# Performance work log

Hardware: AMD Instinct MI355X
Metric: run time of the kernel (lower is better)

## Reference

```python
import jax, jax.numpy as jnp
import numpy as np

B, N, DIN, K, DS = 64, 4096, 256, 20, 64
NUM_ITERS = 3
EPS = 1e-8       # slot-attention eps
EPS_LN = 1e-5    # torch LayerNorm default eps


def _ln(x, g, b):
    m = x.mean(-1, keepdims=True)
    v = ((x - m) ** 2).mean(-1, keepdims=True)
    return (x - m) / jnp.sqrt(v + EPS_LN) * g + b


def setup_inputs() -> dict:
    key = jax.random.key(0)
    ks = jax.random.split(key, 12)
    s = 0.02
    return {
        "inputs": jax.random.normal(ks[0], (B, N, DIN), jnp.float32),
        "slot_noise": jax.random.normal(ks[1], (B, K, DS), jnp.float32),
        "slot_mu": jax.random.normal(ks[2], (1, 1, DS), jnp.float32),
        "slot_log_sigma": jnp.zeros((1, 1, DS), jnp.float32),
        "ln_in_g": jnp.ones((DIN,), jnp.float32),
        "ln_in_b": jnp.zeros((DIN,), jnp.float32),
        "Wk": jax.random.normal(ks[3], (DIN, DS), jnp.float32) * s,
        "Wv": jax.random.normal(ks[4], (DIN, DS), jnp.float32) * s,
        "Wq": jax.random.normal(ks[5], (DS, DS), jnp.float32) * s,
        "ln_slot_g": jnp.ones((DS,), jnp.float32),
        "ln_slot_b": jnp.zeros((DS,), jnp.float32),
        "gru_Wih": jax.random.normal(ks[6], (3 * DS, DS), jnp.float32) * s,
        "gru_Whh": jax.random.normal(ks[7], (3 * DS, DS), jnp.float32) * s,
        "gru_bih": jnp.zeros((3 * DS,), jnp.float32),
        "gru_bhh": jnp.zeros((3 * DS,), jnp.float32),
        "ln_mlp_g": jnp.ones((DS,), jnp.float32),
        "ln_mlp_b": jnp.zeros((DS,), jnp.float32),
        "mlp_W1": jax.random.normal(ks[8], (DS, 4 * DS), jnp.float32) * s,
        "mlp_b1": jnp.zeros((4 * DS,), jnp.float32),
        "mlp_W2": jax.random.normal(ks[9], (4 * DS, DS), jnp.float32) * s,
        "mlp_b2": jnp.zeros((DS,), jnp.float32),
    }


def reference(inputs, slot_noise, slot_mu, slot_log_sigma, ln_in_g, ln_in_b,
              Wk, Wv, Wq, ln_slot_g, ln_slot_b,
              gru_Wih, gru_Whh, gru_bih, gru_bhh,
              ln_mlp_g, ln_mlp_b, mlp_W1, mlp_b1, mlp_W2, mlp_b2):
    x = _ln(inputs, ln_in_g, ln_in_b)            # (B, N, DIN)
    k = x @ Wk                                    # (B, N, DS)
    v = x @ Wv                                    # (B, N, DS)
    slots = slot_mu + jnp.exp(slot_log_sigma) * slot_noise  # (B, K, DS)
    scale = DS ** -0.5
    attn = None
    for _ in range(NUM_ITERS):
        slots_prev = slots
        q = _ln(slots, ln_slot_g, ln_slot_b) @ Wq                # (B, K, DS)
        dots = jnp.einsum('bkd,bnd->bkn', q, k) * scale          # (B, K, N)
        attn = jax.nn.softmax(dots, axis=1)                      # softmax over slots
        attn_norm = attn / (attn.sum(-1, keepdims=True) + EPS)
        updates = jnp.einsum('bkn,bnd->bkd', attn_norm, v)       # (B, K, DS)
        # torch GRUCell: gates ordered r, z, n
        gi = updates @ gru_Wih.T + gru_bih
        gh = slots_prev @ gru_Whh.T + gru_bhh
        i_r, i_z, i_n = jnp.split(gi, 3, axis=-1)
        h_r, h_z, h_n = jnp.split(gh, 3, axis=-1)
        r = jax.nn.sigmoid(i_r + h_r)
        z = jax.nn.sigmoid(i_z + h_z)
        n = jnp.tanh(i_n + r * h_n)
        slots = (1.0 - z) * n + z * slots_prev
        h = _ln(slots, ln_mlp_g, ln_mlp_b)
        slots = slots + (jax.nn.relu(h @ mlp_W1 + mlp_b1) @ mlp_W2 + mlp_b2)
    return slots, attn
```

## Files before the change

kernel.cpp:

```cpp
#include <hip/hip_runtime.h>
#include <cstdint>
#include <cstddef>

using f32x4  = __attribute__((ext_vector_type(4))) float;
using bf16x8 = __attribute__((ext_vector_type(8))) short;

__device__ __forceinline__ unsigned short f2bf(float f){
  unsigned int u = __float_as_uint(f);
  return (unsigned short)((u + 0x7fffu + ((u >> 16) & 1u)) >> 16);
}

#define SWZ(o)    ((o) ^ ((((o) >> 9) & 7) << 4))
#define SWZ128(o) ((o) ^ ((((o) >> 7) & 7) << 4))

__global__ __launch_bounds__(256) void k_prep(
    const float* __restrict__ Wk, const float* __restrict__ Wv,
    const float* __restrict__ Wih, const float* __restrict__ Whh,
    const float* __restrict__ W1,  const float* __restrict__ W2,
    const float* __restrict__ Wq,
    const float* __restrict__ noise, const float* __restrict__ mu,
    const float* __restrict__ lsig,
    const float* __restrict__ lsg, const float* __restrict__ lsb,
    unsigned short* __restrict__ PWt,
    unsigned short* __restrict__ PWih, unsigned short* __restrict__ PWhh,
    unsigned short* __restrict__ PW1T, unsigned short* __restrict__ PW2T,
    unsigned short* __restrict__ PWq,
    float* __restrict__ slots, float* __restrict__ qws){
  const int bx = blockIdx.x, t = threadIdx.x;
  if (bx < 128){
    int idx = bx * 256 + t;
    int e = idx & 7, lane = (idx >> 3) & 63, f = idx >> 9;
    int pass = f >> 5, brT = (f >> 3) & 3, kk = f & 7;
    int n_loc = brT * 16 + (lane & 15);
    int c = kk * 32 + (lane >> 4) * 8 + e;
    const float* src = pass ? Wv : Wk;
    PWt[idx] = f2bf(src[c * 64 + n_loc]);
    return;
  }
  if (bx < 368){
    int idx = (bx - 128) * 256 + t;
    int rel, kstN;
    const float* src; unsigned short* dst; int mode;
    if (idx < 12288)      { rel = idx;          kstN = 2; src = Wih; dst = PWih; mode = 0; }
    else if (idx < 24576) { rel = idx - 12288;  kstN = 2; src = Whh; dst = PWhh; mode = 0; }
    else if (idx < 40960) { rel = idx - 24576;  kstN = 2; src = W1;  dst = PW1T; mode = 1; }
    else if (idx < 57344) { rel = idx - 40960;  kstN = 8; src = W2;  dst = PW2T; mode = 2; }
    else                  { rel = idx - 57344;  kstN = 2; src = Wq;  dst = PWq;  mode = 3; }
    int e = rel & 7, lane = (rel >> 3) & 63, f = rel >> 9;
    int jt = f / kstN, kst = f - jt * kstN;
    int row = jt * 16 + (lane & 15);
    int col = kst * 32 + (lane >> 4) * 8 + e;
    float v;
    if (mode == 0)      v = src[row * 64 + col];
    else if (mode == 1) v = src[col * 256 + row];
    else if (mode == 2) v = src[col * 64 + row];
    else                v = src[col * 64 + row];
    dst[rel] = f2bf(v);
    return;
  }
  {
    __shared__ __align__(16) float xsh[4][64];
    int idx = bx - 368;
    int d = t & 63, w4 = t >> 6;
    int bk = idx * 4 + w4;
    float s = mu[d] + __expf(lsig[d]) * noise[bk * 64 + d];
    slots[bk * 64 + d] = s;
    float s1 = s, s2 = s * s;
    #pragma unroll
    for (int off = 32; off >= 1; off >>= 1){
      s1 += __shfl_xor(s1, off);
      s2 += __shfl_xor(s2, off);
    }
    float m = s1 * (1.f / 64.f);
    float var = s2 * (1.f / 64.f) - m * m;
    float rstd = rsqrtf(var + 1e-5f);
    float xn = (s - m) * rstd * lsg[d] + lsb[d];
    xsh[w4][d] = xn;
    __syncthreads();
    float q = 0.f;
    #pragma unroll
    for (int i = 0; i < 64; ++i) q += xsh[w4][i] * Wq[i * 64 + d];
    qws[bk * 64 + d] = q;
  }
}

__global__ __launch_bounds__(256) void k_lnkv(
    const float* __restrict__ x, const float* __restrict__ lng, const float* __restrict__ lnb,
    const unsigned short* __restrict__ PWt,
    unsigned short* __restrict__ kbF, unsigned short* __restrict__ vF){
  extern __shared__ char smem[];
  char* As = smem;
  char* Cs = smem + 16384;
  const int t = threadIdx.x;
  const int lane = t & 63, w = t >> 6;
  const int gm0 = blockIdx.x * 32;

  const float4 g4 = *(const float4*)(lng + lane * 4);
  const float4 b4 = *(const float4*)(lnb + lane * 4);

  {
    float4 xv[8];
    #pragma unroll
    for (int j = 0; j < 8; ++j){
      int r = w * 8 + j;
      xv[j] = *(const float4*)(x + (size_t)(gm0 + r) * 256 + lane * 4);
    }
    #pragma unroll
    for (int j = 0; j < 8; ++j){
      int r = w * 8 + j;
      float4 v = xv[j];
      float s  = v.x + v.y + v.z + v.w;
      float s2 = v.x * v.x + v.y * v.y + v.z * v.z + v.w * v.w;
      #pragma unroll
      for (int off = 32; off >= 1; off >>= 1){
        s  += __shfl_xor(s,  off);
        s2 += __shfl_xor(s2, off);
      }
      float mean = s * (1.f / 256.f);
      float var  = s2 * (1.f / 256.f) - mean * mean;
      float rstd = rsqrtf(var + 1e-5f);
      unsigned int p0 = (unsigned)f2bf((v.x - mean) * rstd * g4.x + b4.x) |
                        ((unsigned)f2bf((v.y - mean) * rstd * g4.y + b4.y) << 16);
      unsigned int p1 = (unsigned)f2bf((v.z - mean) * rstd * g4.z + b4.z) |
                        ((unsigned)f2bf((v.w - mean) * rstd * g4.w + b4.w) << 16);
      int off8 = r * 512 + lane * 8;
      *(uint2*)(As + SWZ(off8)) = make_uint2(p0, p1);
    }
  }
  __syncthreads();

  const int wm = w >> 1, wn = w & 1;
  const int l15 = lane & 15, l4 = lane >> 4;

  #pragma unroll 1
  for (int pass = 0; pass < 2; ++pass){
    f32x4 acc[2];
    acc[0] = (f32x4){0.f,0.f,0.f,0.f};
    acc[1] = (f32x4){0.f,0.f,0.f,0.f};

    #pragma unroll
    for (int kk = 0; kk < 8; ++kk){
      int ar = wm * 16 + l15;
      bf16x8 a = *(const bf16x8*)(As + SWZ(ar * 512 + kk * 64 + l4 * 16));
      bf16x8 bfr[2];
      #pragma unroll
      for (int j = 0; j < 2; ++j){
        int f = pass * 32 + (wn * 2 + j) * 8 + kk;
        bfr[j] = *(const bf16x8*)(PWt + ((size_t)(f * 64 + lane)) * 8);
      }
      #pragma unroll
      for (int j = 0; j < 2; ++j)
        acc[j] = __builtin_amdgcn_mfma_f32_16x16x32_bf16(a, bfr[j], acc[j], 0, 0, 0);
    }
    if (pass == 1) __syncthreads();

    #pragma unroll
    for (int j = 0; j < 2; ++j)
      #pragma unroll
      for (int reg = 0; reg < 4; ++reg){
        int row = wm * 16 + l4 * 4 + reg;
        int colb = ((wn * 2 + j) * 16 + l15) * 2;
        *(unsigned short*)(Cs + row * 128 + (colb ^ ((row & 7) << 4))) = f2bf(acc[j][reg]);
      }
    __syncthreads();

    if (pass == 0){
      const int lo = t & 63, kst = (t >> 6) & 1, nt = t >> 7;
      int row = nt * 16 + (lo & 15);
      int colb = (kst * 32 + (lo >> 4) * 8) * 2;
      uint4 val = *(const uint4*)(Cs + row * 128 + (colb ^ ((row & 7) << 4)));
      size_t ntile = (size_t)blockIdx.x * 2 + nt;
      *(uint4*)(kbF + (ntile * 2 + kst) * 512 + lo * 8) = val;
    } else {
      const size_t chunkF = (size_t)(gm0 >> 7);
      const int kstG = (gm0 >> 5) & 3;
      const int dtile = t >> 6;
      unsigned short ev[8];
      #pragma unroll
      for (int e = 0; e < 8; ++e){
        int row = (lane >> 4) * 8 + e;
        int colb = (dtile * 16 + (lane & 15)) * 2;
        ev[e] = *(const unsigned short*)(Cs + row * 128 + (colb ^ ((row & 7) << 4)));
      }
      *(uint4*)(vF + ((chunkF * 4 + dtile) * 4 + kstG) * 512 + lane * 8) = *(const uint4*)ev;
    }
  }
}

__global__ __launch_bounds__(256) void k_attn2(
    const unsigned short* __restrict__ kbF, const unsigned short* __restrict__ vF,
    const float* __restrict__ qws, float* __restrict__ Spart, float* __restrict__ Upart,
    float* __restrict__ attn_out, int write_attn){
  __shared__ __align__(16) char sm[12672];
  char* qs  = sm;
  char* Ps  = sm + 4096;
  float* sred = (float*)(sm + 12288);
  const int t = threadIdx.x, lane = t & 63, w = t >> 6;
  const int l15 = lane & 15, g = lane >> 4;
  const int b = blockIdx.y, chunk = blockIdx.x, n0 = chunk * 128;

  if (t < 160){
    int r = t >> 3, c = t & 7;
    const float4* qp = (const float4*)(qws + (size_t)b * 1280 + r * 64 + c * 8);
    float4 a0 = qp[0], a1 = qp[1];
    uint4 pk;
    pk.x = (unsigned)f2bf(a0.x) | ((unsigned)f2bf(a0.y) << 16);
    pk.y = (unsigned)f2bf(a0.z) | ((unsigned)f2bf(a0.w) << 16);
    pk.z = (unsigned)f2bf(a1.x) | ((unsigned)f2bf(a1.y) << 16);
    pk.w = (unsigned)f2bf(a1.z) | ((unsigned)f2bf(a1.w) << 16);
    *(uint4*)(qs + r * 128 + ((c * 16) ^ ((r & 7) << 4))) = pk;
  }
  __syncthreads();

  f32x4 c2[2][2];
  #pragma unroll
  for (int kt = 0; kt < 2; ++kt)
    #pragma unroll
    for (int nt = 0; nt < 2; ++nt)
      c2[kt][nt] = (f32x4){0.f, 0.f, 0.f, 0.f};
  #pragma unroll
  for (int kst = 0; kst < 2; ++kst){
    bf16x8 aq[2], bk2[2];
    #pragma unroll
    for (int kt = 0; kt < 2; ++kt){
      int row = kt * 16 + l15;
      aq[kt] = *(const bf16x8*)(qs + row * 128 + ((kst * 64 + g * 16) ^ ((row & 7) << 4)));
    }
    #pragma unroll
    for (int nt = 0; nt < 2; ++nt){
      size_t ntile = (size_t)b * 256 + chunk * 8 + w * 2 + nt;
      bk2[nt] = *(const bf16x8*)(kbF + (ntile * 2 + kst) * 512 + lane * 8);
    }
    #pragma unroll
    for (int kt = 0; kt < 2; ++kt)
      #pragma unroll
      for (int nt = 0; nt < 2; ++nt)
        c2[kt][nt] = __builtin_amdgcn_mfma_f32_16x16x32_bf16(aq[kt], bk2[nt], c2[kt][nt], 0, 0, 0);
  }

  float p[2][2][4];
  #pragma unroll
  for (int kt = 0; kt < 2; ++kt)
    #pragma unroll
    for (int nt = 0; nt < 2; ++nt)
      #pragma unroll
      for (int reg = 0; reg < 4; ++reg)
        p[kt][nt][reg] = c2[kt][nt][reg] * 0.125f;
  if (g){
    #pragma unroll
    for (int nt = 0; nt < 2; ++nt)
      #pragma unroll
      for (int reg = 0; reg < 4; ++reg)
        p[1][nt][reg] = -1e30f;
  }

  #pragma unroll
  for (int nt = 0; nt < 2; ++nt){
    float mx = p[0][nt][0];
    #pragma unroll
    for (int reg = 1; reg < 4; ++reg) mx = fmaxf(mx, p[0][nt][reg]);
    #pragma unroll
    for (int reg = 0; reg < 4; ++reg) mx = fmaxf(mx, p[1][nt][reg]);
    mx = fmaxf(mx, __shfl_xor(mx, 16));
    mx = fmaxf(mx, __shfl_xor(mx, 32));
    float s = 0.f;
    #pragma unroll
    for (int kt = 0; kt < 2; ++kt)
      #pragma unroll
      for (int reg = 0; reg < 4; ++reg){
        float e = __expf(p[kt][nt][reg] - mx);
        p[kt][nt][reg] = e; s += e;
      }
    s += __shfl_xor(s, 16);
    s += __shfl_xor(s, 32);
    float inv = 1.f / s;
    #pragma unroll
    for (int kt = 0; kt < 2; ++kt)
      #pragma unroll
      for (int reg = 0; reg < 4; ++reg)
        p[kt][nt][reg] *= inv;
  }

  {
    float sr[2][4];
    #pragma unroll
    for (int kt = 0; kt < 2; ++kt)
      #pragma unroll
      for (int reg = 0; reg < 4; ++reg)
        sr[kt][reg] = p[kt][0][reg] + p[kt][1][reg];
    #pragma unroll
    for (int off = 1; off <= 8; off <<= 1)
      #pragma unroll
      for (int kt = 0; kt < 2; ++kt)
        #pragma unroll
        for (int reg = 0; reg < 4; ++reg)
          sr[kt][reg] += __shfl_xor(sr[kt][reg], off);
    if (l15 == 0){
      #pragma unroll
      for (int kt = 0; kt < 2; ++kt)
        #pragma unroll
        for (int reg = 0; reg < 4; ++reg){
          int ks = kt * 16 + g * 4 + reg;
          if (ks < 20) sred[ks * 4 + w] = sr[kt][reg];
        }
    }
  }

  if (write_attn){
    #pragma unroll
    for (int kt = 0; kt < 2; ++kt)
      #pragma unroll
      for (int nt = 0; nt < 2; ++nt)
        #pragma unroll
        for (int reg = 0; reg < 4; ++reg){
          int ks = kt * 16 + g * 4 + reg;
          if (ks < 20)
            attn_out[((size_t)(b * 20 + ks)) * 4096 + n0 + w * 32 + nt * 16 + l15] = p[kt][nt][reg];
        }
  }

  #pragma unroll
  for (int kt = 0; kt < 2; ++kt)
    #pragma unroll
    for (int nt = 0; nt < 2; ++nt)
      #pragma unroll
      for (int reg = 0; reg < 4; ++reg){
        int row = kt * 16 + g * 4 + reg;
        int colb = (w * 32 + nt * 16 + l15) * 2;
        *(unsigned short*)(Ps + row * 256 + (colb ^ ((row & 7) << 4))) = f2bf(p[kt][nt][reg]);
      }
  __syncthreads();

  if (t < 20)
    Spart[((size_t)b * 20 + t) * 32 + chunk] =
        sred[t * 4 + 0] + sred[t * 4 + 1] + sred[t * 4 + 2] + sred[t * 4 + 3];

  f32x4 u[2];
  u[0] = (f32x4){0.f,0.f,0.f,0.f};
  u[1] = (f32x4){0.f,0.f,0.f,0.f};
  #pragma unroll
  for (int kst = 0; kst < 4; ++kst){
    bf16x8 pa[2], bv;
    #pragma unroll
    for (int kt = 0; kt < 2; ++kt){
      int row = kt * 16 + l15;
      pa[kt] = *(const bf16x8*)(Ps + row * 256 + ((kst * 64 + g * 16) ^ ((row & 7) << 4)));
    }
    bv = *(const bf16x8*)(vF + ((((size_t)b * 32 + chunk) * 4 + w) * 4 + kst) * 512 + lane * 8);
    #pragma unroll
    for (int kt = 0; kt < 2; ++kt)
      u[kt] = __builtin_amdgcn_mfma_f32_16x16x32_bf16(pa[kt], bv, u[kt], 0, 0, 0);
  }
  #pragma unroll
  for (int kt = 0; kt < 2; ++kt)
    #pragma unroll
    for (int reg = 0; reg < 4; ++reg){
      int ks = kt * 16 + g * 4 + reg;
      if (ks < 20)
        Upart[((size_t)(b * 32 + chunk) * 20 + ks) * 64 + w * 16 + l15] = u[kt][reg];
    }
}

__global__ __launch_bounds__(1024) void k_slot(
    float* __restrict__ slots, const float* __restrict__ Upart, const float* __restrict__ Spart,
    const unsigned short* __restrict__ PWih, const unsigned short* __restrict__ PWhh,
    const unsigned short* __restrict__ PW1T, const unsigned short* __restrict__ PW2T,
    const unsigned short* __restrict__ PWq,
    const float* __restrict__ bih, const float* __restrict__ bhh,
    const float* __restrict__ b1, const float* __restrict__ b2,
    const float* __restrict__ lmg, const float* __restrict__ lmb,
    const float* __restrict__ lsg, const float* __restrict__ lsb,
    float* __restrict__ qws, float* __restrict__ out_slots, int last){
  extern __shared__ char sm[];
  float* g1f = (float*)sm;
  float* g2f = g1f + 192 * 33;
  char*  reluT = sm;
  char*  ubf   = sm + 50688;
  char*  sbfb  = sm + 54784;
  char*  hbf   = sm + 58880;
  char*  sqbf  = sm + 62976;
  float* snewF = (float*)(sm + 67072);
  float* prevF = (float*)(sm + 75392);
  float* sfinF = (float*)(sm + 83712);
  float* sSr   = (float*)(sm + 92032);

  const int t = threadIdx.x, lane = t & 63, wv = t >> 6;
  const int l15 = lane & 15, g4 = lane >> 4;
  const int b = blockIdx.x;

  if (t < 20){
    const float* sp = Spart + ((size_t)b * 20 + t) * 32;
    float ss = 0.f;
    #pragma unroll
    for (int c = 0; c < 32; ++c) ss += sp[c];
    sSr[t] = 1.f / (ss + 1e-8f);
  }
  __syncthreads();

  #pragma unroll
  for (int i = 0; i < 2; ++i){
    int idx = t + 1024 * i;
    if (idx < 1280){
      int m = idx >> 6, d = idx & 63;
      const float* up = Upart + (size_t)b * 40960 + m * 64 + d;
      float uv = 0.f;
      #pragma unroll
      for (int c = 0; c < 32; ++c) uv += up[(size_t)c * 1280];
      uv *= sSr[m];
      float pv = slots[((size_t)b * 20 + m) * 64 + d];
      int off = m * 128 + d * 2;
      *(unsigned short*)(ubf  + SWZ128(off)) = f2bf(uv);
      *(unsigned short*)(sbfb + SWZ128(off)) = f2bf(pv);
      prevF[m * 65 + d] = pv;
    }
  }
  __syncthreads();

  {
    const int which = wv >> 3, mg = (wv >> 2) & 1, jg = wv & 3;
    const unsigned short* PA = which ? PWhh : PWih;
    const char* Bt = which ? sbfb : ubf;
    float* gout = which ? g2f : g1f;
    f32x4 acc[3];
    #pragma unroll
    for (int jj = 0; jj < 3; ++jj) acc[jj] = (f32x4){0.f,0.f,0.f,0.f};
    #pragma unroll
    for (int kst = 0; kst < 2; ++kst){
      int roff = (mg * 16 + l15) * 128 + (kst * 32 + g4 * 8) * 2;
      bf16x8 bfrag = *(const bf16x8*)(Bt + SWZ128(roff));
      #pragma unroll
      for (int jj = 0; jj < 3; ++jj){
        int jt = jg * 3 + jj;
        bf16x8 afrag = *(const bf16x8*)(PA + ((size_t)((jt * 2 + kst) * 64 + lane)) * 8);
        acc[jj] = __builtin_amdgcn_mfma_f32_16x16x32_bf16(afrag, bfrag, acc[jj], 0, 0, 0);
      }
    }
    #pragma unroll
    for (int jj = 0; jj < 3; ++jj){
      int jt = jg * 3 + jj;
      #pragma unroll
      for (int reg = 0; reg < 4; ++reg)
        gout[(jt * 16 + g4 * 4 + reg) * 33 + mg * 16 + l15] = acc[jj][reg];
    }
  }
  __syncthreads();

  {
    const int d = lane;
    const float bi_r = bih[d], bi_z = bih[64 + d], bi_n = bih[128 + d];
    const float bh_r = bhh[d], bh_z = bhh[64 + d], bh_n = bhh[128 + d];
    const float lg = lmg[d], lb = lmb[d];
    #pragma unroll
    for (int mi = 0; mi < 2; ++mi){
      int m = wv + mi * 16;
      if (m < 20){
        float i_r = g1f[d * 33 + m] + bi_r;
        float i_z = g1f[(64 + d) * 33 + m] + bi_z;
        float i_n = g1f[(128 + d) * 33 + m] + bi_n;
        float h_r = g2f[d * 33 + m] + bh_r;
        float h_z = g2f[(64 + d) * 33 + m] + bh_z;
        float h_n = g2f[(128 + d) * 33 + m] + bh_n;
        float r = 1.f / (1.f + __expf(-(i_r + h_r)));
        float z = 1.f / (1.f + __expf(-(i_z + h_z)));
        float nn = tanhf(i_n + r * h_n);
        float pv = prevF[m * 65 + d];
        float sn = (1.f - z) * nn + z * pv;
        snewF[m * 65 + d] = sn;
        float s1 = sn, s2 = sn * sn;
        #pragma unroll
        for (int off = 32; off >= 1; off >>= 1){
          s1 += __shfl_xor(s1, off);
          s2 += __shfl_xor(s2, off);
        }
        float mean = s1 * (1.f / 64.f);
        float var = s2 * (1.f / 64.f) - mean * mean;
        float rstd = rsqrtf(var + 1e-5f);
        float h = (sn - mean) * rstd * lg + lb;
        *(unsigned short*)(hbf + SWZ128(m * 128 + d * 2)) = f2bf(h);
      }
    }
  }
  __syncthreads();

  {
    const int jt = wv;
    f32x4 acc[2];
    acc[0] = (f32x4){0.f,0.f,0.f,0.f};
    acc[1] = (f32x4){0.f,0.f,0.f,0.f};
    #pragma unroll
    for (int kst = 0; kst < 2; ++kst){
      bf16x8 afrag = *(const bf16x8*)(PW1T + ((size_t)((jt * 2 + kst) * 64 + lane)) * 8);
      #pragma unroll
      for (int mg = 0; mg < 2; ++mg){
        int roff = (mg * 16 + l15) * 128 + (kst * 32 + g4 * 8) * 2;
        bf16x8 bh2 = *(const bf16x8*)(hbf + SWZ128(roff));
        acc[mg] = __builtin_amdgcn_mfma_f32_16x16x32_bf16(afrag, bh2, acc[mg], 0, 0, 0);
      }
    }
    #pragma unroll
    for (int reg = 0; reg < 4; ++reg){
      int j = jt * 16 + g4 * 4 + reg;
      float bb = b1[j];
      #pragma unroll
      for (int mg = 0; mg < 2; ++mg){
        float vv = fmaxf(acc[mg][reg] + bb, 0.f);
        int m = mg * 16 + l15;
        int off = m * 512 + j * 2;
        *(unsigned short*)(reluT + SWZ(off)) = f2bf(vv);
      }
    }
  }
  __syncthreads();

  if (wv < 8){
    const int dd = wv >> 1, mg = wv & 1;
    f32x4 acc = (f32x4){0.f,0.f,0.f,0.f};
    #pragma unroll
    for (int kst = 0; kst < 8; ++kst){
      bf16x8 afrag = *(const bf16x8*)(PW2T + ((size_t)((dd * 8 + kst) * 64 + lane)) * 8);
      int row = mg * 16 + l15;
      int off = row * 512 + (kst * 32 + g4 * 8) * 2;
      bf16x8 bfrag = *(const bf16x8*)(reluT + SWZ(off));
      acc = __builtin_amdgcn_mfma_f32_16x16x32_bf16(afrag, bfrag, acc, 0, 0, 0);
    }
    #pragma unroll
    for (int reg = 0; reg < 4; ++reg){
      int m = mg * 16 + l15;
      int dcol = dd * 16 + g4 * 4 + reg;
      if (m < 20){
        float sf = snewF[m * 65 + dcol] + acc[reg] + b2[dcol];
        sfinF[m * 65 + dcol] = sf;
        slots[((size_t)b * 20 + m) * 64 + dcol] = sf;
        if (last) out_slots[((size_t)b * 20 + m) * 64 + dcol] = sf;
      }
    }
  }
  if (last) return;
  __syncthreads();

  {
    const int d = lane;
    const float lg = lsg[d], lb = lsb[d];
    #pragma unroll
    for (int mi = 0; mi < 2; ++mi){
      int m = wv + mi * 16;
      if (m < 20){
        float sv = sfinF[m * 65 + d];
        float s1 = sv, s2 = sv * sv;
        #pragma unroll
        for (int off = 32; off >= 1; off >>= 1){
          s1 += __shfl_xor(s1, off);
          s2 += __shfl_xor(s2, off);
        }
        float mean = s1 * (1.f / 64.f);
        float var = s2 * (1.f / 64.f) - mean * mean;
        float rstd = rsqrtf(var + 1e-5f);
        float xn = (sv - mean) * rstd * lg + lb;
        *(unsigned short*)(sqbf + SWZ128(m * 128 + d * 2)) = f2bf(xn);
      }
    }
  }
  __syncthreads();
  if (wv < 8){
    const int jt = wv >> 1, mg = wv & 1;
    f32x4 acc = (f32x4){0.f,0.f,0.f,0.f};
    #pragma unroll
    for (int kst = 0; kst < 2; ++kst){
      bf16x8 afrag = *(const bf16x8*)(PWq + ((size_t)((jt * 2 + kst) * 64 + lane)) * 8);
      int roff = (mg * 16 + l15) * 128 + (kst * 32 + g4 * 8) * 2;
      bf16x8 bfrag = *(const bf16x8*)(sqbf + SWZ128(roff));
      acc = __builtin_amdgcn_mfma_f32_16x16x32_bf16(afrag, bfrag, acc, 0, 0, 0);
    }
    #pragma unroll
    for (int reg = 0; reg < 4; ++reg){
      int m = mg * 16 + l15;
      int j = jt * 16 + g4 * 4 + reg;
      if (m < 20) qws[(size_t)b * 1280 + m * 64 + j] = acc[reg];
    }
  }
}

extern "C" void kernel_launch(void* const* d_in, const int* in_sizes, int n_in,
                              void* d_out, int out_size, void* d_ws, size_t ws_size,
                              hipStream_t stream){
  const float* inputs = (const float*)d_in[0];
  const float* noise  = (const float*)d_in[1];
  const float* mu     = (const float*)d_in[2];
  const float* lsig   = (const float*)d_in[3];
  const float* ln_in_g= (const float*)d_in[4];
  const float* ln_in_b= (const float*)d_in[5];
  const float* Wk     = (const float*)d_in[6];
  const float* Wv     = (const float*)d_in[7];
  const float* Wq     = (const float*)d_in[8];
  const float* ln_s_g = (const float*)d_in[9];
  const float* ln_s_b = (const float*)d_in[10];
  const float* Wih    = (const float*)d_in[11];
  const float* Whh    = (const float*)d_in[12];
  const float* bih    = (const float*)d_in[13];
  const float* bhh    = (const float*)d_in[14];
  const float* lmg    = (const float*)d_in[15];
  const float* lmb    = (const float*)d_in[16];
  const float* W1     = (const float*)d_in[17];
  const float* b1     = (const float*)d_in[18];
  const float* W2     = (const float*)d_in[19];
  const float* b2     = (const float*)d_in[20];

  char* ws = (char*)d_ws;
  unsigned short* kbF = (unsigned short*)ws;
  unsigned short* vF  = (unsigned short*)(ws + 33554432);
  unsigned short* PWt = (unsigned short*)(ws + 67108864);
  float* slots        = (float*)(ws + 67174400);
  float* qws          = (float*)(ws + 67502080);
  float* Upart        = (float*)(ws + 67829760);
  float* Spart        = (float*)(ws + 78315520);
  unsigned short* PWih= (unsigned short*)(ws + 78479360);
  unsigned short* PWhh= (unsigned short*)(ws + 78503936);
  unsigned short* PW1T= (unsigned short*)(ws + 78528512);
  unsigned short* PW2T= (unsigned short*)(ws + 78561280);
  unsigned short* PWq = (unsigned short*)(ws + 78594048);

  float* slots_out = (float*)d_out;
  float* attn_out  = slots_out + 81920;

  hipLaunchKernelGGL(k_prep, dim3(688), dim3(256), 0, stream,
                     Wk, Wv, Wih, Whh, W1, W2, Wq, noise, mu, lsig, ln_s_g, ln_s_b,
                     PWt, PWih, PWhh, PW1T, PW2T, PWq, slots, qws);
  hipLaunchKernelGGL(k_lnkv, dim3(8192), dim3(256), 20480, stream, inputs, ln_in_g, ln_in_b,
                     PWt, kbF, vF);

  for (int it = 0; it < 3; ++it){
    hipLaunchKernelGGL(k_attn2, dim3(32, 64), dim3(256), 0, stream, kbF, vF, qws, Spart, Upart,
                       attn_out, (it == 2) ? 1 : 0);
    hipLaunchKernelGGL(k_slot, dim3(64), dim3(1024), 92160, stream, slots, Upart, Spart,
                       PWih, PWhh, PW1T, PW2T, PWq, bih, bhh, b1, b2,
                       lmg, lmb, ln_s_g, ln_s_b, qws, slots_out, (it == 2) ? 1 : 0);
  }
}
```

Before: 164.4 us.

## Replace per-chunk partial sums with atomic accumulation and fold small prep into lnkv

The attention kernel now accumulates slot sums and updates with float atomicAdd into a compact per-batch buffer instead of writing 32 per-chunk partials, and the slot kernel reads and zeroes that buffer. This removes the 32-way partial reduction reads in k_slot and the large partial-buffer traffic. The GRU/MLP weight packing and initial slot/q computation move into extra blocks of the k_lnkv launch, so the prep kernel becomes small and also zeroes the accumulators. Atomics add contention (32 chunks per address) and make the summation order nondeterministic.

```diff
diff --git a/kernel.cpp b/kernel.cpp
--- a/kernel.cpp
+++ b/kernel.cpp
@@ -15,85 +15,93 @@
 
 __global__ __launch_bounds__(256) void k_prep(
     const float* __restrict__ Wk, const float* __restrict__ Wv,
+    unsigned short* __restrict__ PWt, float* __restrict__ Uacc ){
+  const int bx = blockIdx.x, t = threadIdx.x;
+  int idx = bx * 256 + t;
+  int e = idx & 7, lane = (idx >> 3) & 63, f = idx >> 9;
+  int pass = f >> 5, brT = (f >> 3) & 3, kk = f & 7;
+  int n_loc = brT * 16 + (lane & 15);
+  int c = kk * 32 + (lane >> 4) * 8 + e;
+  const float* src = pass ? Wv : Wk;
+  PWt[idx] = f2bf(src[c * 64 + n_loc]);
+  #pragma unroll
+  for (int i = 0; i < 3; ++i){
+    int z = idx + 32768 * i;
+    if (z < 83200) Uacc[z] = 0.f;
+  }
+}
+
+__global__ __launch_bounds__(256) void k_lnkv(
+    const float* __restrict__ x, const float* __restrict__ lng, const float* __restrict__ lnb,
+    const unsigned short* __restrict__ PWt,
+    unsigned short* __restrict__ kbF, unsigned short* __restrict__ vF,
     const float* __restrict__ Wih, const float* __restrict__ Whh,
     const float* __restrict__ W1,  const float* __restrict__ W2,
     const float* __restrict__ Wq,
     const float* __restrict__ noise, const float* __restrict__ mu,
     const float* __restrict__ lsig,
     const float* __restrict__ lsg, const float* __restrict__ lsb,
-    unsigned short* __restrict__ PWt,
     unsigned short* __restrict__ PWih, unsigned short* __restrict__ PWhh,
     unsigned short* __restrict__ PW1T, unsigned short* __restrict__ PW2T,
     unsigned short* __restrict__ PWq,
     float* __restrict__ slots, float* __restrict__ qws){
-  const int bx = blockIdx.x, t = threadIdx.x;
-  if (bx < 128){
-    int idx = bx * 256 + t;
-    int e = idx & 7, lane = (idx >> 3) & 63, f = idx >> 9;
-    int pass = f >> 5, brT = (f >> 3) & 3, kk = f & 7;
-    int n_loc = brT * 16 + (lane & 15);
-    int c = kk * 32 + (lane >> 4) * 8 + e;
-    const float* src = pass ? Wv : Wk;
-    PWt[idx] = f2bf(src[c * 64 + n_loc]);
-    return;
-  }
-  if (bx < 368){
-    int idx = (bx - 128) * 256 + t;
-    int rel, kstN;
-    const float* src; unsigned short* dst; int mode;
-    if (idx < 12288)      { rel = idx;          kstN = 2; src = Wih; dst = PWih; mode = 0; }
-    else if (idx < 24576) { rel = idx - 12288;  kstN = 2; src = Whh; dst = PWhh; mode = 0; }
-    else if (idx < 40960) { rel = idx - 24576;  kstN = 2; src = W1;  dst = PW1T; mode = 1; }
-    else if (idx < 57344) { rel = idx - 40960;  kstN = 8; src = W2;  dst = PW2T; mode = 2; }
-    else                  { rel = idx - 57344;  kstN = 2; src = Wq;  dst = PWq;  mode = 3; }
-    int e = rel & 7, lane = (rel >> 3) & 63, f = rel >> 9;
-    int jt = f / kstN, kst = f - jt * kstN;
-    int row = jt * 16 + (lane & 15);
-    int col = kst * 32 + (lane >> 4) * 8 + e;
-    float v;
-    if (mode == 0)      v = src[row * 64 + col];
-    else if (mode == 1) v = src[col * 256 + row];
-    else if (mode == 2) v = src[col * 64 + row];
-    else                v = src[col * 64 + row];
-    dst[rel] = f2bf(v);
-    return;
-  }
-  {
-    __shared__ __align__(16) float xsh[4][64];
-    int idx = bx - 368;
-    int d = t & 63, w4 = t >> 6;
-    int bk = idx * 4 + w4;
-    float s = mu[d] + __expf(lsig[d]) * noise[bk * 64 + d];
-    slots[bk * 64 + d] = s;
-    float s1 = s, s2 = s * s;
-    #pragma unroll
-    for (int off = 32; off >= 1; off >>= 1){
-      s1 += __shfl_xor(s1, off);
-      s2 += __shfl_xor(s2, off);
-    }
-    float m = s1 * (1.f / 64.f);
-    float var = s2 * (1.f / 64.f) - m * m;
-    float rstd = rsqrtf(var + 1e-5f);
-    float xn = (s - m) * rstd * lsg[d] + lsb[d];
-    xsh[w4][d] = xn;
-    __syncthreads();
-    float q = 0.f;
-    #pragma unroll
-    for (int i = 0; i < 64; ++i) q += xsh[w4][i] * Wq[i * 64 + d];
-    qws[bk * 64 + d] = q;
-  }
-}
-
-__global__ __launch_bounds__(256) void k_lnkv(
-    const float* __restrict__ x, const float* __restrict__ lng, const float* __restrict__ lnb,
-    const unsigned short* __restrict__ PWt,
-    unsigned short* __restrict__ kbF, unsigned short* __restrict__ vF){
   extern __shared__ char smem[];
+  const int t = threadIdx.x;
+  const int bx = blockIdx.x;
+
+  if (bx >= 8192){
+    if (bx < 8432){
+      int idx = (bx - 8192) * 256 + t;
+      int rel, kstN;
+      const float* src; unsigned short* dst; int mode;
+      if (idx < 12288)      { rel = idx;          kstN = 2; src = Wih; dst = PWih; mode = 0; }
+      else if (idx < 24576) { rel = idx - 12288;  kstN = 2; src = Whh; dst = PWhh; mode = 0; }
+      else if (idx < 40960) { rel = idx - 24576;  kstN = 2; src = W1;  dst = PW1T; mode = 1; }
+      else if (idx < 57344) { rel = idx - 40960;  kstN = 8; src = W2;  dst = PW2T; mode = 2; }
+      else                  { rel = idx - 57344;  kstN = 2; src = Wq;  dst = PWq;  mode = 3; }
+      int e = rel & 7, lane = (rel >> 3) & 63, f = rel >> 9;
+      int jt = f / kstN, kst = f - jt * kstN;
+      int row = jt * 16 + (lane & 15);
+      int col = kst * 32 + (lane >> 4) * 8 + e;
+      float v;
+      if (mode == 0)      v = src[row * 64 + col];
+      else if (mode == 1) v = src[col * 256 + row];
+      else if (mode == 2) v = src[col * 64 + row];
+      else                v = src[col * 64 + row];
+      dst[rel] = f2bf(v);
+      return;
+    }
+    {
+      float* xsh = (float*)smem;
+      int idx = bx - 8432;
+      int d = t & 63, w4 = t >> 6;
+      int bk = idx * 4 + w4;
+      float s = mu[d] + __expf(lsig[d]) * noise[bk * 64 + d];
+      slots[bk * 64 + d] = s;
+      float s1 = s, s2 = s * s;
+      #pragma unroll
+      for (int off = 32; off >= 1; off >>= 1){
+        s1 += __shfl_xor(s1, off);
+        s2 += __shfl_xor(s2, off);
+      }
+      float m = s1 * (1.f / 64.f);
+      float var = s2 * (1.f / 64.f) - m * m;
+      float rstd = rsqrtf(var + 1e-5f);
+      float xn = (s - m) * rstd * lsg[d] + lsb[d];
+      xsh[w4 * 64 + d] = xn;
+      __syncthreads();
+      float q = 0.f;
+      #pragma unroll
+      for (int i = 0; i < 64; ++i) q += xsh[w4 * 64 + i] * Wq[i * 64 + d];
+      qws[bk * 64 + d] = q;
+      return;
+    }
+  }
+
   char* As = smem;
   char* Cs = smem + 16384;
-  const int t = threadIdx.x;
   const int lane = t & 63, w = t >> 6;
-  const int gm0 = blockIdx.x * 32;
+  const int gm0 = bx * 32;
 
   const float4 g4 = *(const float4*)(lng + lane * 4);
   const float4 b4 = *(const float4*)(lnb + lane * 4);
@@ -169,7 +177,7 @@
       int row = nt * 16 + (lo & 15);
       int colb = (kst * 32 + (lo >> 4) * 8) * 2;
       uint4 val = *(const uint4*)(Cs + row * 128 + (colb ^ ((row & 7) << 4)));
-      size_t ntile = (size_t)blockIdx.x * 2 + nt;
+      size_t ntile = (size_t)bx * 2 + nt;
       *(uint4*)(kbF + (ntile * 2 + kst) * 512 + lo * 8) = val;
     } else {
       const size_t chunkF = (size_t)(gm0 >> 7);
@@ -189,7 +197,7 @@
 
 __global__ __launch_bounds__(256) void k_attn2(
     const unsigned short* __restrict__ kbF, const unsigned short* __restrict__ vF,
-    const float* __restrict__ qws, float* __restrict__ Spart, float* __restrict__ Upart,
+    const float* __restrict__ qws, float* __restrict__ Sacc, float* __restrict__ Uacc,
     float* __restrict__ attn_out, int write_attn){
   __shared__ __align__(16) char sm[12672];
   char* qs  = sm;
@@ -332,8 +340,8 @@
   __syncthreads();
 
   if (t < 20)
-    Spart[((size_t)b * 20 + t) * 32 + chunk] =
-        sred[t * 4 + 0] + sred[t * 4 + 1] + sred[t * 4 + 2] + sred[t * 4 + 3];
+    atomicAdd(Sacc + (size_t)b * 20 + t,
+              sred[t * 4 + 0] + sred[t * 4 + 1] + sred[t * 4 + 2] + sred[t * 4 + 3]);
 
   f32x4 u[2];
   u[0] = (f32x4){0.f,0.f,0.f,0.f};
@@ -357,12 +365,12 @@
     for (int reg = 0; reg < 4; ++reg){
       int ks = kt * 16 + g * 4 + reg;
       if (ks < 20)
-        Upart[((size_t)(b * 32 + chunk) * 20 + ks) * 64 + w * 16 + l15] = u[kt][reg];
+        atomicAdd(Uacc + (size_t)b * 1280 + ks * 64 + w * 16 + l15, u[kt][reg]);
     }
 }
 
 __global__ __launch_bounds__(1024) void k_slot(
-    float* __restrict__ slots, const float* __restrict__ Upart, const float* __restrict__ Spart,
+    float* __restrict__ slots, float* __restrict__ Uacc, float* __restrict__ Sacc,
     const unsigned short* __restrict__ PWih, const unsigned short* __restrict__ PWhh,
     const unsigned short* __restrict__ PW1T, const unsigned short* __restrict__ PW2T,
     const unsigned short* __restrict__ PWq,
@@ -389,10 +397,8 @@
   const int b = blockIdx.x;
 
   if (t < 20){
-    const float* sp = Spart + ((size_t)b * 20 + t) * 32;
-    float ss = 0.f;
-    #pragma unroll
-    for (int c = 0; c < 32; ++c) ss += sp[c];
+    float ss = Sacc[(size_t)b * 20 + t];
+    Sacc[(size_t)b * 20 + t] = 0.f;
     sSr[t] = 1.f / (ss + 1e-8f);
   }
   __syncthreads();
@@ -402,10 +408,8 @@
     int idx = t + 1024 * i;
     if (idx < 1280){
       int m = idx >> 6, d = idx & 63;
-      const float* up = Upart + (size_t)b * 40960 + m * 64 + d;
-      float uv = 0.f;
-      #pragma unroll
-      for (int c = 0; c < 32; ++c) uv += up[(size_t)c * 1280];
+      float uv = Uacc[(size_t)b * 1280 + idx];
+      Uacc[(size_t)b * 1280 + idx] = 0.f;
       uv *= sSr[m];
       float pv = slots[((size_t)b * 20 + m) * 64 + d];
       int off = m * 128 + d * 2;
@@ -611,27 +615,27 @@
   unsigned short* PWt = (unsigned short*)(ws + 67108864);
   float* slots        = (float*)(ws + 67174400);
   float* qws          = (float*)(ws + 67502080);
-  float* Upart        = (float*)(ws + 67829760);
-  float* Spart        = (float*)(ws + 78315520);
-  unsigned short* PWih= (unsigned short*)(ws + 78479360);
-  unsigned short* PWhh= (unsigned short*)(ws + 78503936);
-  unsigned short* PW1T= (unsigned short*)(ws + 78528512);
-  unsigned short* PW2T= (unsigned short*)(ws + 78561280);
-  unsigned short* PWq = (unsigned short*)(ws + 78594048);
+  float* Uacc         = (float*)(ws + 67829760);
+  float* Sacc         = (float*)(ws + 68157440);
+  unsigned short* PWih= (unsigned short*)(ws + 68162560);
+  unsigned short* PWhh= (unsigned short*)(ws + 68187136);
+  unsigned short* PW1T= (unsigned short*)(ws + 68211712);
+  unsigned short* PW2T= (unsigned short*)(ws + 68244480);
+  unsigned short* PWq = (unsigned short*)(ws + 68277248);
 
   float* slots_out = (float*)d_out;
   float* attn_out  = slots_out + 81920;
 
-  hipLaunchKernelGGL(k_prep, dim3(688), dim3(256), 0, stream,
-                     Wk, Wv, Wih, Whh, W1, W2, Wq, noise, mu, lsig, ln_s_g, ln_s_b,
-                     PWt, PWih, PWhh, PW1T, PW2T, PWq, slots, qws);
-  hipLaunchKernelGGL(k_lnkv, dim3(8192), dim3(256), 20480, stream, inputs, ln_in_g, ln_in_b,
-                     PWt, kbF, vF);
+  hipLaunchKernelGGL(k_prep, dim3(128), dim3(256), 0, stream, Wk, Wv, PWt, Uacc);
+  hipLaunchKernelGGL(k_lnkv, dim3(8752), dim3(256), 20480, stream, inputs, ln_in_g, ln_in_b,
+                     PWt, kbF, vF,
+                     Wih, Whh, W1, W2, Wq, noise, mu, lsig, ln_s_g, ln_s_b,
+                     PWih, PWhh, PW1T, PW2T, PWq, slots, qws);
 
   for (int it = 0; it < 3; ++it){
-    hipLaunchKernelGGL(k_attn2, dim3(32, 64), dim3(256), 0, stream, kbF, vF, qws, Spart, Upart,
+    hipLaunchKernelGGL(k_attn2, dim3(32, 64), dim3(256), 0, stream, kbF, vF, qws, Sacc, Uacc,
                        attn_out, (it == 2) ? 1 : 0);
-    hipLaunchKernelGGL(k_slot, dim3(64), dim3(1024), 92160, stream, slots, Upart, Spart,
+    hipLaunchKernelGGL(k_slot, dim3(64), dim3(1024), 92160, stream, slots, Uacc, Sacc,
                        PWih, PWhh, PW1T, PW2T, PWq, bih, bhh, b1, b2,
                        lmg, lmb, ln_s_g, ln_s_b, qws, slots_out, (it == 2) ? 1 : 0);
   }
```

Result: slower. 185.0 us (+12.5%).
